# Optimization experiments

Hardware: AMD Instinct MI355X
Metric: run time of the kernel (lower is better)

The kernel has to match this reference:

```python
import jax, jax.numpy as jnp
import numpy as np

IGNORE_INDEX = -100
CHUNK = 256  # tokens per chunk; avoids materializing full [N, V] logits


def _fused_linear_ce_mean(hidden, weight, labels):
    # hidden: [N, H] float, weight: [V, H] float, labels: [N] int
    N, H = hidden.shape
    pad = (-N) % CHUNK
    h = jnp.pad(hidden, ((0, pad), (0, 0)))
    l = jnp.pad(labels, (0, pad), constant_values=IGNORE_INDEX)
    h = h.reshape(-1, CHUNK, H)
    l = l.reshape(-1, CHUNK)

    def body(args):
        hc, lc = args                      # [CHUNK, H], [CHUNK]
        logits = hc @ weight.T             # [CHUNK, V] — only chunk-sized
        lse = jax.nn.logsumexp(logits, axis=-1)
        idx = jnp.clip(lc, 0)[:, None]
        tgt = jnp.take_along_axis(logits, idx, axis=-1)[:, 0]
        valid = lc != IGNORE_INDEX
        nll = jnp.where(valid, lse - tgt, 0.0)
        return nll, valid

    nll, valid = jax.lax.map(body, (h, l))
    return nll.sum() / valid.sum()


def setup_inputs() -> dict:
    key = jax.random.key(0)
    k1, k2, k3 = jax.random.split(key, 3)
    B, S, H, V = 1, 2048, 2048, 151936
    hidden_states = jax.random.normal(k1, (B, S, H), dtype=jnp.float32)
    labels = jax.random.randint(k2, (B, S), 0, V, dtype=jnp.int64)
    weight = jax.random.normal(k3, (V, H), dtype=jnp.float32) * 0.02
    return {"hidden_states": hidden_states, "labels": labels, "weight": weight}


def reference(hidden_states, labels, weight):
    # shift: predict token t+1 from hidden state t
    shift_hidden = hidden_states[..., :-1, :]            # [B, S-1, H]
    shift_labels = labels[..., 1:]                        # [B, S-1]
    H = shift_hidden.shape[-1]
    flat_h = shift_hidden.reshape(-1, H)
    flat_l = shift_labels.reshape(-1)
    return _fused_linear_ce_mean(flat_h, weight, flat_l)
```

## Files before the change

### kernel.cpp

```cpp
#include <hip/hip_runtime.h>
#include <hip/hip_bf16.h>
#include <math.h>


#define V_SIZE   151936
#define H_SIZE   2048
#define M_ROWS   2048
#define M_REAL   2047
#define NB_CNT   1187
#define BM 128
#define BN 128
#define BK 64
#define NBLK (16 * NB_CNT)
#define IGNORE_INDEX (-100)

typedef short bf16x8 __attribute__((ext_vector_type(8)));
typedef float floatx4 __attribute__((ext_vector_type(4)));

__device__ __forceinline__ unsigned short f2bf_rne(float f) {
    union { float f; unsigned u; } x; x.f = f;
    unsigned r = (x.u + 0x7fffu + ((x.u >> 16) & 1u)) >> 16;
    return (unsigned short)r;
}

__device__ __forceinline__ void gload16(const void* g, void* l) {
    __builtin_amdgcn_global_load_lds(
        (const __attribute__((address_space(1))) unsigned int*)g,
        (__attribute__((address_space(3))) unsigned int*)l, 16, 0, 0);
}


__global__ void cvt_weight(const float4* __restrict__ in,
                           ushort4* __restrict__ out, long n4) {
    long i = (long)blockIdx.x * blockDim.x + threadIdx.x;
    long stride = (long)gridDim.x * blockDim.x;
    for (; i < n4; i += stride) {
        float4 v = in[i];
        ushort4 o;
        o.x = f2bf_rne(v.x); o.y = f2bf_rne(v.y);
        o.z = f2bf_rne(v.z); o.w = f2bf_rne(v.w);
        out[i] = o;
    }
}

__global__ void cvt_hidden(const float4* __restrict__ in,
                           ushort4* __restrict__ out) {
    const long n4 = (long)M_ROWS * H_SIZE / 4;
    const long valid4 = (long)M_REAL * H_SIZE / 4;
    long i = (long)blockIdx.x * blockDim.x + threadIdx.x;
    long stride = (long)gridDim.x * blockDim.x;
    for (; i < n4; i += stride) {
        ushort4 o;
        if (i < valid4) {
            float4 v = in[i];
            o.x = f2bf_rne(v.x); o.y = f2bf_rne(v.y);
            o.z = f2bf_rne(v.z); o.w = f2bf_rne(v.w);
        } else {
            o.x = 0; o.y = 0; o.z = 0; o.w = 0;
        }
        out[i] = o;
    }
}


__global__ __launch_bounds__(256, 4) void gemm_lse(
    const unsigned short* __restrict__ hbf,
    const unsigned short* __restrict__ wbf,
    float* __restrict__ pmax,
    float* __restrict__ psum) {
    __shared__ short ldsA[BM * BK];
    __shared__ short ldsB[BN * BK];
    __shared__ float eM[BM][2];
    __shared__ float eS[BM][2];

    const int t    = threadIdx.x;
    const int lane = t & 63;
    const int w    = t >> 6;
    const int wm   = w >> 1;
    const int wn   = w & 1;

    const int b    = blockIdx.x;
    const int lin  = (b & 7) * (NBLK / 8) + (b >> 3);
    const int mb   = lin & 15;
    const int nb   = lin >> 4;
    const int m0   = mb * BM;
    const int n0   = nb * BN;

    const int srow   = t >> 3;
    const int schunk = (t & 7) ^ (srow & 7);
    const unsigned short* pa = hbf + (size_t)(m0 + srow) * H_SIZE + schunk * 8;
    const unsigned short* pb = wbf + (size_t)(n0 + srow) * H_SIZE + schunk * 8;
    short* la = &ldsA[t * 8];
    short* lb = &ldsB[t * 8];

    floatx4 zero4 = {0.f, 0.f, 0.f, 0.f};
    floatx4 acc[4][4];
#pragma unroll
    for (int i = 0; i < 4; ++i)
#pragma unroll
        for (int j = 0; j < 4; ++j) acc[i][j] = zero4;

    const int fr  = lane & 15;
    const int fq  = lane >> 4;
    const int rsw = fr & 7;

    for (int kt = 0; kt < H_SIZE / BK; ++kt) {
        const int kof = kt * BK;
#pragma unroll
        for (int i = 0; i < 4; ++i) {
            gload16(pa + (size_t)i * 32 * H_SIZE + kof, la + i * 2048);
            gload16(pb + (size_t)i * 32 * H_SIZE + kof, lb + i * 2048);
        }
        __syncthreads();
#pragma unroll
        for (int kk = 0; kk < 2; ++kk) {
            bf16x8 af[4], bfv[4];
#pragma unroll
            for (int i = 0; i < 4; ++i)
                af[i] = *(const bf16x8*)&ldsA[(wm * 64 + i * 16 + fr) * BK
                                              + (((kk * 4 + fq) ^ rsw) * 8)];
#pragma unroll
            for (int j = 0; j < 4; ++j)
                bfv[j] = *(const bf16x8*)&ldsB[(wn * 64 + j * 16 + fr) * BK
                                               + (((kk * 4 + fq) ^ rsw) * 8)];
#pragma unroll
            for (int i = 0; i < 4; ++i)
#pragma unroll
                for (int j = 0; j < 4; ++j)
                    acc[i][j] = __builtin_amdgcn_mfma_f32_16x16x32_bf16(
                        af[i], bfv[j], acc[i][j], 0, 0, 0);
        }
        __syncthreads();
    }

#pragma unroll
    for (int i = 0; i < 4; ++i) {
#pragma unroll
        for (int r = 0; r < 4; ++r) {
            float v = -INFINITY;
#pragma unroll
            for (int j = 0; j < 4; ++j) v = fmaxf(v, acc[i][j][r]);
            for (int off = 1; off < 16; off <<= 1)
                v = fmaxf(v, __shfl_xor(v, off, 64));
            float s = 0.f;
#pragma unroll
            for (int j = 0; j < 4; ++j) s += expf(acc[i][j][r] - v);
            for (int off = 1; off < 16; off <<= 1)
                s += __shfl_xor(s, off, 64);
            if (fr == 0) {
                int row = wm * 64 + i * 16 + fq * 4 + r;
                eM[row][wn] = v;
                eS[row][wn] = s;
            }
        }
    }
    __syncthreads();
    if (t < BM) {
        float ma = eM[t][0], mb2 = eM[t][1];
        float Mx = fmaxf(ma, mb2);
        float Sx = eS[t][0] * expf(ma - Mx) + eS[t][1] * expf(mb2 - Mx);
        size_t grow = (size_t)m0 + t;
        pmax[(size_t)nb * M_ROWS + grow] = Mx;
        psum[(size_t)nb * M_ROWS + grow] = Sx;
    }
}


__global__ void zero_acc(float* a) {
    if (threadIdx.x < 2) a[threadIdx.x] = 0.f;
}

__global__ __launch_bounds__(256) void reduce_rows(
    const float* __restrict__ hid,
    const int* __restrict__ labels,
    const float* __restrict__ wt,
    const float* __restrict__ pmax,
    const float* __restrict__ psum,
    float* __restrict__ accum) {
    const int m = blockIdx.x;
    const int t = threadIdx.x;
    const int lbl = labels[m + 1];
    const bool valid = (lbl != IGNORE_INDEX);

    float dot = 0.f;
    if (valid) {
        int li = lbl < 0 ? 0 : lbl;
        const float4* hr = (const float4*)(hid + (size_t)m * H_SIZE);
        const float4* wr = (const float4*)(wt + (size_t)li * H_SIZE);
#pragma unroll
        for (int i = 0; i < 2; ++i) {
            float4 a = hr[t + i * 256];
            float4 b = wr[t + i * 256];
            dot += a.x * b.x + a.y * b.y + a.z * b.z + a.w * b.w;
        }
    }

    float M = -INFINITY, S = 0.f;
    for (int nbi = t; nbi < NB_CNT; nbi += 256) {
        float m2 = pmax[(size_t)nbi * M_ROWS + m];
        float s2 = psum[(size_t)nbi * M_ROWS + m];
        if (m2 > M) { S = S * expf(M - m2) + s2; M = m2; }
        else        { S += s2 * expf(m2 - M); }
    }
    for (int off = 1; off < 64; off <<= 1) {
        float M2 = __shfl_xor(M, off, 64);
        float S2 = __shfl_xor(S, off, 64);
        float nm = fmaxf(M, M2);
        S = S * expf(M - nm) + S2 * expf(M2 - nm);
        M = nm;
        dot += __shfl_xor(dot, off, 64);
    }
    __shared__ float rM[4], rS[4], rD[4];
    const int wv = t >> 6, lane = t & 63;
    if (lane == 0) { rM[wv] = M; rS[wv] = S; rD[wv] = dot; }
    __syncthreads();
    if (t == 0) {
        float Mx = rM[0], Sx = rS[0], D = rD[0];
        for (int i = 1; i < 4; ++i) {
            float nm = fmaxf(Mx, rM[i]);
            Sx = Sx * expf(Mx - nm) + rS[i] * expf(rM[i] - nm);
            Mx = nm;
            D += rD[i];
        }
        if (valid) {
            atomicAdd(&accum[0], (Mx + logf(Sx)) - D);
            atomicAdd(&accum[1], 1.0f);
        }
    }
}

__global__ void finalize(const float* __restrict__ accum, float* __restrict__ out) {
    out[0] = accum[0] / accum[1];
}

__global__ void sentinel(float* out) { out[0] = -12345.0f; }


extern "C" void kernel_launch(void* const* d_in, const int* in_sizes, int n_in,
                              void* d_out, int out_size, void* d_ws, size_t ws_size,
                              hipStream_t stream) {
    const float* hid    = (const float*)d_in[0];
    const int*   labels = (const int*)d_in[1];
    const float* wt     = (const float*)d_in[2];
    float* out = (float*)d_out;

    const size_t wbf_bytes  = (size_t)V_SIZE * H_SIZE * 2;
    const size_t hbf_bytes  = (size_t)M_ROWS * H_SIZE * 2;
    const size_t part_bytes = (size_t)NB_CNT * M_ROWS * 4;
    const size_t off_wbf  = 0;
    const size_t off_hbf  = off_wbf + wbf_bytes;
    const size_t off_pmax = off_hbf + hbf_bytes;
    const size_t off_psum = off_pmax + part_bytes;
    const size_t off_acc  = off_psum + part_bytes;
    const size_t need     = off_acc + 16;

    if (ws_size < need) {
        sentinel<<<1, 1, 0, stream>>>(out);
        return;
    }

    unsigned short* wbf = (unsigned short*)((char*)d_ws + off_wbf);
    unsigned short* hbf = (unsigned short*)((char*)d_ws + off_hbf);
    float* pmax = (float*)((char*)d_ws + off_pmax);
    float* psum = (float*)((char*)d_ws + off_psum);
    float* accum = (float*)((char*)d_ws + off_acc);

    zero_acc<<<1, 64, 0, stream>>>(accum);

    long w4 = (long)V_SIZE * H_SIZE / 4;
    cvt_weight<<<2048, 256, 0, stream>>>((const float4*)wt, (ushort4*)wbf, w4);
    cvt_hidden<<<1024, 256, 0, stream>>>((const float4*)hid, (ushort4*)hbf);

    gemm_lse<<<NBLK, 256, 0, stream>>>(hbf, wbf, pmax, psum);

    reduce_rows<<<M_REAL, 256, 0, stream>>>(hid, labels, wt, pmax, psum, accum);
    finalize<<<1, 1, 0, stream>>>(accum, out);
}
```

Measured before the change: 1.784 ms.

## Switch logits GEMM from bf16 to fp8 scaled MFMA with weight prescale

```diff
diff --git a/kernel.cpp b/kernel.cpp
--- a/kernel.cpp
+++ b/kernel.cpp
@@ -10,18 +10,17 @@
 #define NB_CNT   1187
 #define BM 128
 #define BN 128
-#define BK 64
+#define BKB 128
+#define KSTEPS (H_SIZE / BKB)
 #define NBLK (16 * NB_CNT)
 #define IGNORE_INDEX (-100)
 
-typedef short bf16x8 __attribute__((ext_vector_type(8)));
+typedef int   i32x4  __attribute__((ext_vector_type(4)));
+typedef int   i32x8  __attribute__((ext_vector_type(8)));
 typedef float floatx4 __attribute__((ext_vector_type(4)));
 
-__device__ __forceinline__ unsigned short f2bf_rne(float f) {
-    union { float f; unsigned u; } x; x.f = f;
-    unsigned r = (x.u + 0x7fffu + ((x.u >> 16) & 1u)) >> 16;
-    return (unsigned short)r;
-}
+#define SCALE_ONE   0x7F7F7F7FU
+#define SCALE_W     0x79797979U
 
 __device__ __forceinline__ void gload16(const void* g, void* l) {
     __builtin_amdgcn_global_load_lds(
@@ -30,33 +29,31 @@
 }
 
 
-__global__ void cvt_weight(const float4* __restrict__ in,
-                           ushort4* __restrict__ out, long n4) {
+__global__ void cvt_w_fp8(const float4* __restrict__ in,
+                          unsigned* __restrict__ out, long n4) {
     long i = (long)blockIdx.x * blockDim.x + threadIdx.x;
     long stride = (long)gridDim.x * blockDim.x;
     for (; i < n4; i += stride) {
         float4 v = in[i];
-        ushort4 o;
-        o.x = f2bf_rne(v.x); o.y = f2bf_rne(v.y);
-        o.z = f2bf_rne(v.z); o.w = f2bf_rne(v.w);
-        out[i] = o;
-    }
-}
-
-__global__ void cvt_hidden(const float4* __restrict__ in,
-                           ushort4* __restrict__ out) {
+        int r = __builtin_amdgcn_cvt_pk_fp8_f32(v.x * 64.f, v.y * 64.f, 0, false);
+        r = __builtin_amdgcn_cvt_pk_fp8_f32(v.z * 64.f, v.w * 64.f, r, true);
+        out[i] = (unsigned)r;
+    }
+}
+
+__global__ void cvt_h_fp8(const float4* __restrict__ in,
+                          unsigned* __restrict__ out) {
     const long n4 = (long)M_ROWS * H_SIZE / 4;
     const long valid4 = (long)M_REAL * H_SIZE / 4;
     long i = (long)blockIdx.x * blockDim.x + threadIdx.x;
     long stride = (long)gridDim.x * blockDim.x;
     for (; i < n4; i += stride) {
-        ushort4 o;
+        unsigned o = 0;
         if (i < valid4) {
             float4 v = in[i];
-            o.x = f2bf_rne(v.x); o.y = f2bf_rne(v.y);
-            o.z = f2bf_rne(v.z); o.w = f2bf_rne(v.w);
-        } else {
-            o.x = 0; o.y = 0; o.z = 0; o.w = 0;
+            int r = __builtin_amdgcn_cvt_pk_fp8_f32(v.x, v.y, 0, false);
+            r = __builtin_amdgcn_cvt_pk_fp8_f32(v.z, v.w, r, true);
+            o = (unsigned)r;
         }
         out[i] = o;
     }
@@ -64,12 +61,12 @@
 
 
 __global__ __launch_bounds__(256, 4) void gemm_lse(
-    const unsigned short* __restrict__ hbf,
-    const unsigned short* __restrict__ wbf,
+    const unsigned char* __restrict__ hq,
+    const unsigned char* __restrict__ wq,
     float* __restrict__ pmax,
     float* __restrict__ psum) {
-    __shared__ short ldsA[BM * BK];
-    __shared__ short ldsB[BN * BK];
+    __shared__ unsigned char ldsA[BM * BKB];
+    __shared__ unsigned char ldsB[BN * BKB];
     __shared__ float eM[BM][2];
     __shared__ float eS[BM][2];
 
@@ -88,10 +85,10 @@
 
     const int srow   = t >> 3;
     const int schunk = (t & 7) ^ (srow & 7);
-    const unsigned short* pa = hbf + (size_t)(m0 + srow) * H_SIZE + schunk * 8;
-    const unsigned short* pb = wbf + (size_t)(n0 + srow) * H_SIZE + schunk * 8;
-    short* la = &ldsA[t * 8];
-    short* lb = &ldsB[t * 8];
+    const unsigned char* gA = hq + (size_t)(m0 + srow) * H_SIZE + schunk * 16;
+    const unsigned char* gB = wq + (size_t)(n0 + srow) * H_SIZE + schunk * 16;
+    unsigned char* la = ldsA + t * 16;
+    unsigned char* lb = ldsB + t * 16;
 
     floatx4 zero4 = {0.f, 0.f, 0.f, 0.f};
     floatx4 acc[4][4];
@@ -100,35 +97,45 @@
 #pragma unroll
         for (int j = 0; j < 4; ++j) acc[i][j] = zero4;
 
-    const int fr  = lane & 15;
-    const int fq  = lane >> 4;
-    const int rsw = fr & 7;
-
-    for (int kt = 0; kt < H_SIZE / BK; ++kt) {
-        const int kof = kt * BK;
+    const int fr = lane & 15;
+    const int fq = lane >> 4;
+    const int sw = fr & 7;
+
+    for (int kt = 0; kt < KSTEPS; ++kt) {
+        const int kof = kt * BKB;
 #pragma unroll
         for (int i = 0; i < 4; ++i) {
-            gload16(pa + (size_t)i * 32 * H_SIZE + kof, la + i * 2048);
-            gload16(pb + (size_t)i * 32 * H_SIZE + kof, lb + i * 2048);
+            gload16(gA + (size_t)i * 32 * H_SIZE + kof, la + i * 4096);
+            gload16(gB + (size_t)i * 32 * H_SIZE + kof, lb + i * 4096);
         }
         __syncthreads();
-#pragma unroll
-        for (int kk = 0; kk < 2; ++kk) {
-            bf16x8 af[4], bfv[4];
+
+        i32x8 af[4];
+#pragma unroll
+        for (int i = 0; i < 4; ++i) {
+            const unsigned char* p = ldsA + (size_t)(wm * 64 + i * 16 + fr) * BKB;
+            i32x4 lo = *(const i32x4*)(p + ((2 * fq) ^ sw) * 16);
+            i32x4 hi = *(const i32x4*)(p + ((2 * fq + 1) ^ sw) * 16);
+            i32x8 a;
+            a[0] = lo[0]; a[1] = lo[1]; a[2] = lo[2]; a[3] = lo[3];
+            a[4] = hi[0]; a[5] = hi[1]; a[6] = hi[2]; a[7] = hi[3];
+            af[i] = a;
+        }
+#pragma unroll
+        for (int j = 0; j < 4; ++j) {
+            const unsigned char* p = ldsB + (size_t)(wn * 64 + j * 16 + fr) * BKB;
+            i32x4 lo = *(const i32x4*)(p + ((2 * fq) ^ sw) * 16);
+            i32x4 hi = *(const i32x4*)(p + ((2 * fq + 1) ^ sw) * 16);
+            i32x8 bfrag;
+            bfrag[0] = lo[0]; bfrag[1] = lo[1]; bfrag[2] = lo[2]; bfrag[3] = lo[3];
+            bfrag[4] = hi[0]; bfrag[5] = hi[1]; bfrag[6] = hi[2]; bfrag[7] = hi[3];
 #pragma unroll
             for (int i = 0; i < 4; ++i)
-                af[i] = *(const bf16x8*)&ldsA[(wm * 64 + i * 16 + fr) * BK
-                                              + (((kk * 4 + fq) ^ rsw) * 8)];
-#pragma unroll
-            for (int j = 0; j < 4; ++j)
-                bfv[j] = *(const bf16x8*)&ldsB[(wn * 64 + j * 16 + fr) * BK
-                                               + (((kk * 4 + fq) ^ rsw) * 8)];
-#pragma unroll
-            for (int i = 0; i < 4; ++i)
-#pragma unroll
-                for (int j = 0; j < 4; ++j)
-                    acc[i][j] = __builtin_amdgcn_mfma_f32_16x16x32_bf16(
-                        af[i], bfv[j], acc[i][j], 0, 0, 0);
+                acc[i][j] = __builtin_amdgcn_mfma_scale_f32_16x16x128_f8f6f4(
+                    af[i], bfrag, acc[i][j],
+                    0, 0,
+                    0, (int)SCALE_ONE,
+                    0, (int)SCALE_W);
         }
         __syncthreads();
     }
@@ -244,12 +251,12 @@
     const float* wt     = (const float*)d_in[2];
     float* out = (float*)d_out;
 
-    const size_t wbf_bytes  = (size_t)V_SIZE * H_SIZE * 2;
-    const size_t hbf_bytes  = (size_t)M_ROWS * H_SIZE * 2;
+    const size_t wq_bytes   = (size_t)V_SIZE * H_SIZE;
+    const size_t hq_bytes   = (size_t)M_ROWS * H_SIZE;
     const size_t part_bytes = (size_t)NB_CNT * M_ROWS * 4;
-    const size_t off_wbf  = 0;
-    const size_t off_hbf  = off_wbf + wbf_bytes;
-    const size_t off_pmax = off_hbf + hbf_bytes;
+    const size_t off_wq   = 0;
+    const size_t off_hq   = off_wq + wq_bytes;
+    const size_t off_pmax = off_hq + hq_bytes;
     const size_t off_psum = off_pmax + part_bytes;
     const size_t off_acc  = off_psum + part_bytes;
     const size_t need     = off_acc + 16;
@@ -259,8 +266,8 @@
         return;
     }
 
-    unsigned short* wbf = (unsigned short*)((char*)d_ws + off_wbf);
-    unsigned short* hbf = (unsigned short*)((char*)d_ws + off_hbf);
+    unsigned char* wq = (unsigned char*)((char*)d_ws + off_wq);
+    unsigned char* hq = (unsigned char*)((char*)d_ws + off_hq);
     float* pmax = (float*)((char*)d_ws + off_pmax);
     float* psum = (float*)((char*)d_ws + off_psum);
     float* accum = (float*)((char*)d_ws + off_acc);
@@ -268,10 +275,10 @@
     zero_acc<<<1, 64, 0, stream>>>(accum);
 
     long w4 = (long)V_SIZE * H_SIZE / 4;
-    cvt_weight<<<2048, 256, 0, stream>>>((const float4*)wt, (ushort4*)wbf, w4);
-    cvt_hidden<<<1024, 256, 0, stream>>>((const float4*)hid, (ushort4*)hbf);
-
-    gemm_lse<<<NBLK, 256, 0, stream>>>(hbf, wbf, pmax, psum);
+    cvt_w_fp8<<<2048, 256, 0, stream>>>((const float4*)wt, (unsigned*)wq, w4);
+    cvt_h_fp8<<<1024, 256, 0, stream>>>((const float4*)hid, (unsigned*)hq);
+
+    gemm_lse<<<NBLK, 256, 0, stream>>>(hq, wq, pmax, psum);
 
     reduce_rows<<<M_REAL, 256, 0, stream>>>(hid, labels, wt, pmax, psum, accum);
     finalize<<<1, 1, 0, stream>>>(accum, out);
```

After: 5.787 ms. 3.24x slower.
